# Kernel optimization log

Measured on AMD Instinct MI355X. Metric: run time of the kernel, lower is better.

Reference implementation:

```python
import jax, jax.numpy as jnp
import numpy as np

D_MODEL = 1024
N_HEAD = 8
STRIDE = 8
HEAD_DIM = D_MODEL // N_HEAD
NEG_INF = jnp.float32(-1e30)  # stand-in for -inf, safe under softmax


def setup_inputs() -> dict:
    key = jax.random.key(0)
    ks = jax.random.split(key, 8)
    B, TGT, SRC = 2, 1024, 8192
    scale = 1.0 / np.sqrt(D_MODEL)
    return {
        "q": jax.random.normal(ks[0], (B, TGT, D_MODEL), jnp.float32),
        "k": jax.random.normal(ks[1], (B, SRC, D_MODEL), jnp.float32),
        "v": jax.random.normal(ks[2], (B, SRC, D_MODEL), jnp.float32),
        "Wq": jax.random.normal(ks[3], (D_MODEL, D_MODEL), jnp.float32) * scale,
        "bq": jnp.zeros((D_MODEL,), jnp.float32),
        "Wk": jax.random.normal(ks[4], (D_MODEL, D_MODEL), jnp.float32) * scale,
        "bk": jnp.zeros((D_MODEL,), jnp.float32),
        "Wv": jax.random.normal(ks[5], (D_MODEL, D_MODEL), jnp.float32) * scale,
        "bv": jnp.zeros((D_MODEL,), jnp.float32),
        "Wo": jax.random.normal(ks[6], (D_MODEL, D_MODEL), jnp.float32) * scale,
        "bo": jnp.zeros((D_MODEL,), jnp.float32),
    }


def _hepos_head_mask(src_len):
    # mask_h[h, j] True where position j is DISALLOWED for head h:
    # (j - h) % stride != 0. If a head would mask everything, unmask j=0
    # (matches the torch fallback; cannot happen when n_head <= stride... it
    # can when h >= stride? here h < n_head <= stride handled generically).
    src_idx = jnp.arange(src_len)  # [src]
    h_idx = jnp.arange(N_HEAD)[:, None]  # [H,1]
    m = ((src_idx[None, :] - h_idx) % STRIDE) != 0  # [H, src]
    all_masked = jnp.all(m, axis=-1, keepdims=True)  # [H,1]
    m = m.at[:, 0].set(jnp.where(all_masked[:, 0], False, m[:, 0]))
    return m


def reference(q, k, v, Wq, bq, Wk, bk, Wv, bv, Wo, bo):
    B, tgt_len, _ = q.shape
    src_len = k.shape[1]
    # projections (torch Linear: x @ W^T + b; here W stored as [d_in, d_out])
    Q = (q @ Wq + bq).reshape(B, tgt_len, N_HEAD, HEAD_DIM)
    K = (k @ Wk + bk).reshape(B, src_len, N_HEAD, HEAD_DIM)
    V = (v @ Wv + bv).reshape(B, src_len, N_HEAD, HEAD_DIM)
    # dense scores [B, H, tgt, src]
    scores = jnp.einsum('bthd,bshd->bhts', Q, K) / np.sqrt(HEAD_DIM)
    head_mask = _hepos_head_mask(src_len)  # [H, src], True -> disallowed
    scores = jnp.where(head_mask[None, :, None, :], NEG_INF, scores)
    attn = jax.nn.softmax(scores, axis=-1)
    out = jnp.einsum('bhts,bshd->bthd', attn, V).reshape(B, tgt_len, D_MODEL)
    return out @ Wo + bo
```

## Files before the change

kernel.cpp:

```cpp
#include <hip/hip_runtime.h>
#include <hip/hip_bf16.h>
#include <stdint.h>

#define DM 1024
#define HD 128
#define NH 8
#define NB 2
#define TGT 1024
#define SRC 8192
#define JPH 1024
#define LOG2E 1.4426950408889634f

typedef __attribute__((ext_vector_type(8))) short bf16x8;
typedef __attribute__((ext_vector_type(4))) float f32x4;

__device__ __forceinline__ unsigned short f2bf(float f) {
  __hip_bfloat16 h = __float2bfloat16(f);
  return __builtin_bit_cast(unsigned short, h);
}

__device__ __forceinline__ void gload_lds16(const void* g, void* l) {
  __builtin_amdgcn_global_load_lds(
      (const __attribute__((address_space(1))) unsigned int*)g,
      (__attribute__((address_space(3))) unsigned int*)l, 16, 0, 0);
}

__global__ __launch_bounds__(256) void wconv_kernel(
    const float* __restrict__ Wq, const float* __restrict__ Wk,
    const float* __restrict__ Wv, const float* __restrict__ Wo,
    unsigned short* __restrict__ WTout) {
  __shared__ float tile[64][65];
  const float* W = (blockIdx.z == 0) ? Wq : (blockIdx.z == 1) ? Wk
                   : (blockIdx.z == 2) ? Wv : Wo;
  unsigned short* WT = WTout + (size_t)blockIdx.z * DM * DM;
  const int k0 = blockIdx.x * 64, n0 = blockIdx.y * 64;
  const int tid = threadIdx.x;
  const int tr = tid >> 4, tc = (tid & 15) * 4;
  for (int it = 0; it < 4; ++it) {
    int r = tr + it * 16;
    float4 vv = *(const float4*)(&W[(size_t)(k0 + r) * DM + n0 + tc]);
    tile[r][tc] = vv.x; tile[r][tc + 1] = vv.y;
    tile[r][tc + 2] = vv.z; tile[r][tc + 3] = vv.w;
  }
  __syncthreads();
  for (int it = 0; it < 4; ++it) {
    int n = tr + it * 16;
    ushort4 o;
    o.x = f2bf(tile[tc + 0][n]); o.y = f2bf(tile[tc + 1][n]);
    o.z = f2bf(tile[tc + 2][n]); o.w = f2bf(tile[tc + 3][n]);
    *(ushort4*)(&WT[(size_t)(n0 + n) * DM + k0 + tc]) = o;
  }
}

__global__ __launch_bounds__(256, 4) void proj_fused_kernel(
    const float* __restrict__ q, const float* __restrict__ k,
    const float* __restrict__ v, const unsigned short* __restrict__ WTall,
    const float* __restrict__ bq, const float* __restrict__ bk,
    const float* __restrict__ bv, unsigned short* __restrict__ Qp,
    unsigned short* __restrict__ Kp, unsigned short* __restrict__ VpT) {
  __shared__ unsigned short Ab[2][32 * 64];
  __shared__ unsigned short Bb[2][128 * 64];
  const int tid = threadIdx.x, lane = tid & 63, w = tid >> 6;
  const int wm = w >> 1, wn = w & 1;
  const int l15 = lane & 15, l4 = lane >> 4;

  const int bid = blockIdx.x;
  const int lbid = (bid & 7) * 192 + (bid >> 3);
  const int mode = lbid >> 9;
  const int sub = lbid & 511;
  const float* Asrc;
  const unsigned short* WT;
  const float* bias;
  int nbase, bh = 0, Mtile;
  if (mode == 0) {
    Asrc = q; WT = WTall; bias = bq;
    Mtile = sub >> 3; nbase = (sub & 7) * 128;
  } else {
    bh = sub >> 5; Mtile = sub & 31;
    nbase = (bh & 7) * 128;
    if (mode == 1) { Asrc = k; WT = WTall + (size_t)DM * DM; bias = bk; }
    else           { Asrc = v; WT = WTall + (size_t)2 * DM * DM; bias = bv; }
  }

  const int ar = tid >> 3;
  const int ac = (tid & 7) * 8;
  size_t growA;
  if (mode == 0) growA = (size_t)(Mtile * 32 + ar);
  else growA = (size_t)(bh >> 3) * SRC + (size_t)(bh & 7) +
               8u * (size_t)(Mtile * 32 + ar);
  const float* aptr = &Asrc[growA * DM + ac];

  auto issueA = [&](int t, float4 (&R)[2]) {
    const float* src = aptr + t * 64;
    R[0] = *(const float4*)(src);
    R[1] = *(const float4*)(src + 4);
  };
  auto commitA = [&](float4 (&R)[2], int buf) {
    bf16x8 pk;
    pk[0] = (short)f2bf(R[0].x); pk[1] = (short)f2bf(R[0].y);
    pk[2] = (short)f2bf(R[0].z); pk[3] = (short)f2bf(R[0].w);
    pk[4] = (short)f2bf(R[1].x); pk[5] = (short)f2bf(R[1].y);
    pk[6] = (short)f2bf(R[1].z); pk[7] = (short)f2bf(R[1].w);
    int b0 = ar * 128 + ((ac * 2) ^ ((ar & 7) << 4));
    *(bf16x8*)((unsigned char*)Ab[buf] + b0) = pk;
  };
  auto stageB = [&](int t, int buf) {
    const int kk0 = t * 64;
#pragma unroll
    for (int it = 0; it < 4; ++it) {
      int gi = w * 4 + it;
      int row = gi * 8 + (lane >> 3);
      const unsigned char* g =
          (const unsigned char*)&WT[(size_t)(nbase + row) * DM + kk0];
      g += ((lane & 7) * 16) ^ ((row & 7) << 4);
      gload_lds16(g, (unsigned char*)Bb[buf] + gi * 1024);
    }
  };

  f32x4 acc[4] = {};
  float4 aR0[2], aR1[2];

  stageB(0, 0);
  issueA(0, aR0);
  commitA(aR0, 0);
  issueA(1, aR1);
  asm volatile("s_waitcnt vmcnt(2) lgkmcnt(0)" ::: "memory");
  __builtin_amdgcn_s_barrier();
  __builtin_amdgcn_sched_barrier(0);

  auto body = [&](int T, int CUR, float4 (&RC)[2], float4 (&RN)[2]) {
    if (T + 1 < 16) stageB(T + 1, CUR ^ 1);
    if (T + 2 < 16) issueA(T + 2, RC);

    bf16x8 af[2], bfr[4][2];
#pragma unroll
    for (int kk = 0; kk < 2; ++kk) {
      int ra = wm * 16 + l15;
      int ka = (kk * 64 + l4 * 16) ^ ((ra & 7) << 4);
      af[kk] = *(const bf16x8*)((const unsigned char*)Ab[CUR] + ra * 128 + ka);
#pragma unroll
      for (int g = 0; g < 4; ++g) {
        int rb = wn * 64 + g * 16 + l15;
        int kb = (kk * 64 + l4 * 16) ^ ((rb & 7) << 4);
        bfr[g][kk] = *(const bf16x8*)((const unsigned char*)Bb[CUR] + rb * 128 + kb);
      }
    }
#pragma unroll
    for (int kk = 0; kk < 2; ++kk)
#pragma unroll
      for (int g = 0; g < 4; ++g)
        acc[g] = __builtin_amdgcn_mfma_f32_16x16x32_bf16(
            af[kk], bfr[g][kk], acc[g], 0, 0, 0);

    if (T + 1 < 16) commitA(RN, CUR ^ 1);

    if (T + 2 < 16)
      asm volatile("s_waitcnt vmcnt(2) lgkmcnt(0)" ::: "memory");
    else
      asm volatile("s_waitcnt vmcnt(0) lgkmcnt(0)" ::: "memory");
    __builtin_amdgcn_s_barrier();
    __builtin_amdgcn_sched_barrier(0);
  };

  for (int tt = 0; tt < 16; tt += 2) {
    body(tt, 0, aR0, aR1);
    body(tt + 1, 1, aR1, aR0);
  }

#pragma unroll
  for (int g = 0; g < 4; ++g) {
    const int mloc = wm * 16 + l4 * 4;
    const int nloc = wn * 64 + g * 16 + l15;
    const float bs = bias[nbase + nloc];
    if (mode == 2) {
      const int d = nloc;
      const int jp = Mtile * 32 + mloc;
      ushort4 o;
      o.x = f2bf(acc[g][0] + bs); o.y = f2bf(acc[g][1] + bs);
      o.z = f2bf(acc[g][2] + bs); o.w = f2bf(acc[g][3] + bs);
      *(ushort4*)(&VpT[((size_t)bh * HD + d) * JPH + jp]) = o;
    } else if (mode == 1) {
      for (int i = 0; i < 4; ++i) {
        int jp = Mtile * 32 + mloc + i;
        Kp[((size_t)bh * JPH + jp) * HD + nloc] = f2bf(acc[g][i] + bs);
      }
    } else {
      for (int i = 0; i < 4; ++i) {
        int mg = Mtile * 32 + mloc + i;
        int bb = mg >> 10, tt2 = mg & 1023;
        int ng = nbase + nloc;
        int h = ng >> 7, d = ng & 127;
        Qp[(((size_t)bb * NH + h) * TGT + tt2) * HD + d] =
            f2bf((acc[g][i] + bs) * 0.08838834764831845f);
      }
    }
  }
}

__global__ __launch_bounds__(256) void attn_kernel(
    const unsigned short* __restrict__ Qp, const unsigned short* __restrict__ Kp,
    const unsigned short* __restrict__ VpT, unsigned short* __restrict__ O) {
  __shared__ unsigned short Klds[2][64 * 128];
  __shared__ unsigned short Vlds[2][128 * 64];
  __shared__ unsigned short Plds[4 * 16 * 64];
  const int tid = threadIdx.x, lane = tid & 63, w = tid >> 6;
  const int bid = blockIdx.x;
  const int lbid = (bid & 7) * 32 + (bid >> 3);
  const int tq = lbid & 15, bh = lbid >> 4;
  const int T0 = tq * 64 + w * 16;
  const int l15 = lane & 15, l4 = lane >> 4;

  bf16x8 qf[4];
  {
    const unsigned short* qrow = &Qp[((size_t)bh * TGT + T0 + l15) * HD];
    for (int kf = 0; kf < 4; ++kf)
      qf[kf] = *(const bf16x8*)(&qrow[kf * 32 + l4 * 8]);
  }

  f32x4 acc_o[8] = {};
  float m_run = -INFINITY, l_run = 0.f;

  const unsigned short* kbh = Kp + (size_t)bh * JPH * HD;
  const unsigned short* vbh = VpT + (size_t)bh * HD * JPH;

  auto stage = [&](int jt, int buf) {
    const int j0 = jt * 64;
#pragma unroll
    for (int it = 0; it < 4; ++it) {
      int rb = w * 16 + it * 4;
      int row = rb + l4;
      const unsigned char* g =
          (const unsigned char*)(kbh + (size_t)(j0 + row) * HD);
      g += (l15 * 16) ^ ((row & 7) << 4);
      gload_lds16(g, &Klds[buf][rb * 128]);
    }
#pragma unroll
    for (int it = 0; it < 4; ++it) {
      int rb = w * 32 + it * 8;
      int d = rb + (lane >> 3);
      const unsigned char* g =
          (const unsigned char*)(vbh + (size_t)d * JPH + j0);
      g += ((lane & 7) * 16) ^ ((d & 7) << 4);
      gload_lds16(g, &Vlds[buf][rb * 64]);
    }
  };

  stage(0, 0);
  asm volatile("s_waitcnt vmcnt(0)" ::: "memory");
  __builtin_amdgcn_s_barrier();
  __builtin_amdgcn_sched_barrier(0);

  for (int jt = 0; jt < 16; ++jt) {
    const int cb = jt & 1;
    if (jt < 15) stage(jt + 1, cb ^ 1);

    f32x4 acc_s[4] = {};
    for (int jf = 0; jf < 4; ++jf) {
      const int j = jf * 16 + l15;
      for (int kf = 0; kf < 4; ++kf) {
        int byteoff = (j * 256 + (kf * 32 + l4 * 8) * 2) ^ ((j & 7) << 4);
        bf16x8 kfr = *(const bf16x8*)((const unsigned char*)Klds[cb] + byteoff);
        acc_s[jf] = __builtin_amdgcn_mfma_f32_16x16x32_bf16(
            kfr, qf[kf], acc_s[jf], 0, 0, 0);
      }
    }

    float pmax = -INFINITY;
    for (int jf = 0; jf < 4; ++jf)
      for (int i = 0; i < 4; ++i) pmax = fmaxf(pmax, acc_s[jf][i]);
    pmax = fmaxf(pmax, __shfl_xor(pmax, 16, 64));
    pmax = fmaxf(pmax, __shfl_xor(pmax, 32, 64));
    const float m_new = fmaxf(m_run, pmax);
    const float alpha = exp2f((m_run - m_new) * LOG2E);
    float psum = 0.f;
    for (int jf = 0; jf < 4; ++jf) {
      float p0 = exp2f((acc_s[jf][0] - m_new) * LOG2E);
      float p1 = exp2f((acc_s[jf][1] - m_new) * LOG2E);
      float p2 = exp2f((acc_s[jf][2] - m_new) * LOG2E);
      float p3 = exp2f((acc_s[jf][3] - m_new) * LOG2E);
      psum += (p0 + p1) + (p2 + p3);
      ushort4 pk;
      pk.x = f2bf(p0); pk.y = f2bf(p1); pk.z = f2bf(p2); pk.w = f2bf(p3);
      int byteoff = (w * 2048 + l15 * 128 + (jf * 16 + l4 * 4) * 2) ^ ((l15 & 7) << 4);
      *(ushort4*)((unsigned char*)Plds + byteoff) = pk;
    }
    psum += __shfl_xor(psum, 16, 64);
    psum += __shfl_xor(psum, 32, 64);
    l_run = l_run * alpha + psum;
    m_run = m_new;

    float alphar[4];
    for (int i = 0; i < 4; ++i)
      alphar[i] = __shfl(alpha, (lane & 48) | (l4 * 4 + i), 64);
    for (int df = 0; df < 8; ++df) {
      acc_o[df][0] *= alphar[0]; acc_o[df][1] *= alphar[1];
      acc_o[df][2] *= alphar[2]; acc_o[df][3] *= alphar[3];
    }

    for (int kf2 = 0; kf2 < 2; ++kf2) {
      int poff = (w * 2048 + l15 * 128 + (kf2 * 32 + l4 * 8) * 2) ^ ((l15 & 7) << 4);
      bf16x8 pf = *(const bf16x8*)((const unsigned char*)Plds + poff);
      for (int df = 0; df < 8; ++df) {
        int d = df * 16 + l15;
        int voff = (d * 128 + (kf2 * 32 + l4 * 8) * 2) ^ ((d & 7) << 4);
        bf16x8 vf = *(const bf16x8*)((const unsigned char*)Vlds[cb] + voff);
        acc_o[df] = __builtin_amdgcn_mfma_f32_16x16x32_bf16(
            pf, vf, acc_o[df], 0, 0, 0);
      }
    }

    asm volatile("s_waitcnt vmcnt(0)" ::: "memory");
    __builtin_amdgcn_s_barrier();
    __builtin_amdgcn_sched_barrier(0);
  }

  const float li = 1.0f / l_run;
  float linv[4];
  for (int i = 0; i < 4; ++i)
    linv[i] = __shfl(li, (lane & 48) | (l4 * 4 + i), 64);

  const int b = bh >> 3, h = bh & 7;
  for (int df = 0; df < 8; ++df)
    for (int i = 0; i < 4; ++i) {
      int t = T0 + l4 * 4 + i;
      int d = df * 16 + l15;
      O[((size_t)b * TGT + t) * DM + h * HD + d] = f2bf(acc_o[df][i] * linv[i]);
    }
}

__global__ __launch_bounds__(256) void oproj_kernel(
    const unsigned short* __restrict__ Oin, const unsigned short* __restrict__ WoT,
    const float* __restrict__ bo, float* __restrict__ out) {
  __shared__ unsigned short Ab[2][64 * 64];
  __shared__ unsigned short Bb[2][128 * 64];
  const int tid = threadIdx.x, lane = tid & 63, w = tid >> 6;
  const int wm = w >> 1, wn = w & 1;
  const int n0 = blockIdx.x * 128, m0 = blockIdx.y * 64;
  const int l15 = lane & 15, l4 = lane >> 4;

  auto stageA = [&](int t, int buf) {
    const int kk0 = t * 64;
#pragma unroll
    for (int it = 0; it < 2; ++it) {
      int gi = w * 2 + it;
      int row = gi * 8 + (lane >> 3);
      const unsigned char* g =
          (const unsigned char*)&Oin[(size_t)(m0 + row) * DM + kk0];
      g += ((lane & 7) * 16) ^ ((row & 7) << 4);
      gload_lds16(g, (unsigned char*)Ab[buf] + gi * 1024);
    }
  };
  auto stageB = [&](int t, int buf) {
    const int kk0 = t * 64;
#pragma unroll
    for (int it = 0; it < 4; ++it) {
      int gi = w * 4 + it;
      int row = gi * 8 + (lane >> 3);
      const unsigned char* g =
          (const unsigned char*)&WoT[(size_t)(n0 + row) * DM + kk0];
      g += ((lane & 7) * 16) ^ ((row & 7) << 4);
      gload_lds16(g, (unsigned char*)Bb[buf] + gi * 1024);
    }
  };

  f32x4 acc[2][4] = {};
  stageA(0, 0);
  stageB(0, 0);
  asm volatile("s_waitcnt vmcnt(0)" ::: "memory");
  __builtin_amdgcn_s_barrier();
  __builtin_amdgcn_sched_barrier(0);

  for (int t = 0; t < 16; ++t) {
    const int cur = t & 1;
    if (t < 15) { stageA(t + 1, cur ^ 1); stageB(t + 1, cur ^ 1); }

    bf16x8 af[2][2], bfr[4][2];
#pragma unroll
    for (int kk = 0; kk < 2; ++kk) {
#pragma unroll
      for (int f = 0; f < 2; ++f) {
        int ra = wm * 32 + f * 16 + l15;
        int ka = (kk * 64 + l4 * 16) ^ ((ra & 7) << 4);
        af[f][kk] = *(const bf16x8*)((const unsigned char*)Ab[cur] + ra * 128 + ka);
      }
#pragma unroll
      for (int g = 0; g < 4; ++g) {
        int rb = wn * 64 + g * 16 + l15;
        int kb = (kk * 64 + l4 * 16) ^ ((rb & 7) << 4);
        bfr[g][kk] = *(const bf16x8*)((const unsigned char*)Bb[cur] + rb * 128 + kb);
      }
    }
#pragma unroll
    for (int kk = 0; kk < 2; ++kk)
#pragma unroll
      for (int f = 0; f < 2; ++f)
#pragma unroll
        for (int g = 0; g < 4; ++g)
          acc[f][g] = __builtin_amdgcn_mfma_f32_16x16x32_bf16(
              af[f][kk], bfr[g][kk], acc[f][g], 0, 0, 0);

    asm volatile("s_waitcnt vmcnt(0) lgkmcnt(0)" ::: "memory");
    __builtin_amdgcn_s_barrier();
    __builtin_amdgcn_sched_barrier(0);
  }

#pragma unroll
  for (int f = 0; f < 2; ++f)
#pragma unroll
    for (int g = 0; g < 4; ++g) {
      int nn = n0 + wn * 64 + g * 16 + l15;
      float bs = bo[nn];
      for (int i = 0; i < 4; ++i) {
        int mm = m0 + wm * 32 + f * 16 + l4 * 4 + i;
        out[(size_t)mm * DM + nn] = acc[f][g][i] + bs;
      }
    }
}

extern "C" void kernel_launch(void* const* d_in, const int* in_sizes, int n_in,
                              void* d_out, int out_size, void* d_ws,
                              size_t ws_size, hipStream_t stream) {
  const float* q  = (const float*)d_in[0];
  const float* k  = (const float*)d_in[1];
  const float* v  = (const float*)d_in[2];
  const float* Wq = (const float*)d_in[3];
  const float* bq = (const float*)d_in[4];
  const float* Wk = (const float*)d_in[5];
  const float* bk = (const float*)d_in[6];
  const float* Wv = (const float*)d_in[7];
  const float* bv = (const float*)d_in[8];
  const float* Wo = (const float*)d_in[9];
  const float* bo = (const float*)d_in[10];
  float* out = (float*)d_out;

  unsigned short* WT  = (unsigned short*)d_ws;
  unsigned short* Qp  = WT + (size_t)4 * DM * DM;
  unsigned short* Kp  = Qp + (size_t)2 * DM * DM;
  unsigned short* VpT = Kp + (size_t)2 * DM * DM;
  unsigned short* Obf = VpT + (size_t)2 * DM * DM;

  hipLaunchKernelGGL(wconv_kernel, dim3(16, 16, 4), dim3(256), 0, stream,
                     Wq, Wk, Wv, Wo, WT);
  hipLaunchKernelGGL(proj_fused_kernel, dim3(1536), dim3(256), 0, stream,
                     q, k, v, WT, bq, bk, bv, Qp, Kp, VpT);
  hipLaunchKernelGGL(attn_kernel, dim3(256), dim3(256), 0, stream,
                     Qp, Kp, VpT, Obf);
  hipLaunchKernelGGL(oproj_kernel, dim3(8, 32), dim3(256), 0, stream,
                     Obf, WT + (size_t)3 * DM * DM, bo, out);
}
```

Before: 103.5 us.

## Double projection M-tile to 64 rows with triple-buffered B staging

The fused QKV projection kernel now computes 64x128 output tiles per block instead of 32x128, so each wave holds two MFMA row fragments and every staged weight tile is reused across twice as many rows. B staging moves from a double to a triple buffer with a two-tile prefetch distance, and the grid is halved to 768 blocks. Occupancy hints drop from 4 to 2 blocks per CU to allow the larger LDS and register footprint. The aim is to cut weight-tile traffic per output and hide more load latency, at the cost of fewer resident waves and fewer blocks to fill the GPU.

```diff
diff --git a/kernel.cpp b/kernel.cpp
--- a/kernel.cpp
+++ b/kernel.cpp
@@ -52,22 +52,22 @@
   }
 }
 
-__global__ __launch_bounds__(256, 4) void proj_fused_kernel(
+__global__ __launch_bounds__(256, 2) void proj_fused_kernel(
     const float* __restrict__ q, const float* __restrict__ k,
     const float* __restrict__ v, const unsigned short* __restrict__ WTall,
     const float* __restrict__ bq, const float* __restrict__ bk,
     const float* __restrict__ bv, unsigned short* __restrict__ Qp,
     unsigned short* __restrict__ Kp, unsigned short* __restrict__ VpT) {
-  __shared__ unsigned short Ab[2][32 * 64];
-  __shared__ unsigned short Bb[2][128 * 64];
+  __shared__ unsigned short Ab[2][64 * 64];
+  __shared__ unsigned short Bb[3][128 * 64];
   const int tid = threadIdx.x, lane = tid & 63, w = tid >> 6;
   const int wm = w >> 1, wn = w & 1;
   const int l15 = lane & 15, l4 = lane >> 4;
 
   const int bid = blockIdx.x;
-  const int lbid = (bid & 7) * 192 + (bid >> 3);
-  const int mode = lbid >> 9;
-  const int sub = lbid & 511;
+  const int lbid = (bid & 7) * 96 + (bid >> 3);
+  const int mode = lbid >> 8;
+  const int sub = lbid & 255;
   const float* Asrc;
   const unsigned short* WT;
   const float* bias;
@@ -76,36 +76,42 @@
     Asrc = q; WT = WTall; bias = bq;
     Mtile = sub >> 3; nbase = (sub & 7) * 128;
   } else {
-    bh = sub >> 5; Mtile = sub & 31;
+    bh = sub >> 4; Mtile = sub & 15;
     nbase = (bh & 7) * 128;
     if (mode == 1) { Asrc = k; WT = WTall + (size_t)DM * DM; bias = bk; }
     else           { Asrc = v; WT = WTall + (size_t)2 * DM * DM; bias = bv; }
   }
 
-  const int ar = tid >> 3;
-  const int ac = (tid & 7) * 8;
+  const int ar = tid >> 2;
+  const int ac = (tid & 3) * 16;
   size_t growA;
-  if (mode == 0) growA = (size_t)(Mtile * 32 + ar);
+  if (mode == 0) growA = (size_t)(Mtile * 64 + ar);
   else growA = (size_t)(bh >> 3) * SRC + (size_t)(bh & 7) +
-               8u * (size_t)(Mtile * 32 + ar);
+               8u * (size_t)(Mtile * 64 + ar);
   const float* aptr = &Asrc[growA * DM + ac];
 
-  auto issueA = [&](int t, float4 (&R)[2]) {
+  auto issueA = [&](int t, float4 (&R)[4]) {
     const float* src = aptr + t * 64;
-    R[0] = *(const float4*)(src);
-    R[1] = *(const float4*)(src + 4);
-  };
-  auto commitA = [&](float4 (&R)[2], int buf) {
-    bf16x8 pk;
-    pk[0] = (short)f2bf(R[0].x); pk[1] = (short)f2bf(R[0].y);
-    pk[2] = (short)f2bf(R[0].z); pk[3] = (short)f2bf(R[0].w);
-    pk[4] = (short)f2bf(R[1].x); pk[5] = (short)f2bf(R[1].y);
-    pk[6] = (short)f2bf(R[1].z); pk[7] = (short)f2bf(R[1].w);
-    int b0 = ar * 128 + ((ac * 2) ^ ((ar & 7) << 4));
-    *(bf16x8*)((unsigned char*)Ab[buf] + b0) = pk;
+#pragma unroll
+    for (int i = 0; i < 4; ++i) R[i] = *(const float4*)(src + i * 4);
+  };
+  auto commitA = [&](float4 (&R)[4], int buf) {
+    unsigned char* abase = (unsigned char*)Ab[buf] + ar * 128;
+#pragma unroll
+    for (int h = 0; h < 2; ++h) {
+      bf16x8 pk;
+      float4 x = R[h * 2], y = R[h * 2 + 1];
+      pk[0] = (short)f2bf(x.x); pk[1] = (short)f2bf(x.y);
+      pk[2] = (short)f2bf(x.z); pk[3] = (short)f2bf(x.w);
+      pk[4] = (short)f2bf(y.x); pk[5] = (short)f2bf(y.y);
+      pk[6] = (short)f2bf(y.z); pk[7] = (short)f2bf(y.w);
+      int b0 = (ac * 2 + h * 16) ^ ((ar & 7) << 4);
+      *(bf16x8*)(abase + b0) = pk;
+    }
   };
   auto stageB = [&](int t, int buf) {
     const int kk0 = t * 64;
+    unsigned char* dst = (unsigned char*)Bb[buf];
 #pragma unroll
     for (int it = 0; it < 4; ++it) {
       int gi = w * 4 + it;
@@ -113,85 +119,102 @@
       const unsigned char* g =
           (const unsigned char*)&WT[(size_t)(nbase + row) * DM + kk0];
       g += ((lane & 7) * 16) ^ ((row & 7) << 4);
-      gload_lds16(g, (unsigned char*)Bb[buf] + gi * 1024);
-    }
-  };
-
-  f32x4 acc[4] = {};
-  float4 aR0[2], aR1[2];
-
+      gload_lds16(g, dst + gi * 1024);
+    }
+  };
+
+  f32x4 acc[2][4] = {};
+  float4 aR0[4], aR1[4];
+
+  issueA(0, aR0);
   stageB(0, 0);
-  issueA(0, aR0);
+  issueA(1, aR1);
+  stageB(1, 1);
   commitA(aR0, 0);
-  issueA(1, aR1);
-  asm volatile("s_waitcnt vmcnt(2) lgkmcnt(0)" ::: "memory");
+  asm volatile("s_waitcnt vmcnt(8) lgkmcnt(0)" ::: "memory");
   __builtin_amdgcn_s_barrier();
   __builtin_amdgcn_sched_barrier(0);
 
-  auto body = [&](int T, int CUR, float4 (&RC)[2], float4 (&RN)[2]) {
-    if (T + 1 < 16) stageB(T + 1, CUR ^ 1);
-    if (T + 2 < 16) issueA(T + 2, RC);
-
-    bf16x8 af[2], bfr[4][2];
+  int bc = 0;
+
+  auto body = [&](int T, float4 (&RC)[4], float4 (&RN)[4]) {
+    int bp = bc + 2; if (bp >= 3) bp -= 3;
+    if (T + 2 < 16) {
+      issueA(T + 2, RC);
+      stageB(T + 2, bp);
+    }
+
+    const unsigned char* Bbase = (const unsigned char*)Bb[0] + bc * 16384;
+    const unsigned char* Abase = (const unsigned char*)Ab[T & 1];
+    bf16x8 af[2][2], bfr[4][2];
 #pragma unroll
     for (int kk = 0; kk < 2; ++kk) {
-      int ra = wm * 16 + l15;
-      int ka = (kk * 64 + l4 * 16) ^ ((ra & 7) << 4);
-      af[kk] = *(const bf16x8*)((const unsigned char*)Ab[CUR] + ra * 128 + ka);
+#pragma unroll
+      for (int f = 0; f < 2; ++f) {
+        int ra = wm * 32 + f * 16 + l15;
+        int ka = (kk * 64 + l4 * 16) ^ ((ra & 7) << 4);
+        af[f][kk] = *(const bf16x8*)(Abase + ra * 128 + ka);
+      }
 #pragma unroll
       for (int g = 0; g < 4; ++g) {
         int rb = wn * 64 + g * 16 + l15;
         int kb = (kk * 64 + l4 * 16) ^ ((rb & 7) << 4);
-        bfr[g][kk] = *(const bf16x8*)((const unsigned char*)Bb[CUR] + rb * 128 + kb);
+        bfr[g][kk] = *(const bf16x8*)(Bbase + rb * 128 + kb);
       }
     }
 #pragma unroll
     for (int kk = 0; kk < 2; ++kk)
 #pragma unroll
-      for (int g = 0; g < 4; ++g)
-        acc[g] = __builtin_amdgcn_mfma_f32_16x16x32_bf16(
-            af[kk], bfr[g][kk], acc[g], 0, 0, 0);
-
-    if (T + 1 < 16) commitA(RN, CUR ^ 1);
+      for (int f = 0; f < 2; ++f)
+#pragma unroll
+        for (int g = 0; g < 4; ++g)
+          acc[f][g] = __builtin_amdgcn_mfma_f32_16x16x32_bf16(
+              af[f][kk], bfr[g][kk], acc[f][g], 0, 0, 0);
+
+    if (T + 1 < 16) commitA(RN, (T + 1) & 1);
 
     if (T + 2 < 16)
-      asm volatile("s_waitcnt vmcnt(2) lgkmcnt(0)" ::: "memory");
+      asm volatile("s_waitcnt vmcnt(8) lgkmcnt(0)" ::: "memory");
     else
       asm volatile("s_waitcnt vmcnt(0) lgkmcnt(0)" ::: "memory");
     __builtin_amdgcn_s_barrier();
     __builtin_amdgcn_sched_barrier(0);
+    bc = bc + 1; if (bc >= 3) bc -= 3;
   };
 
   for (int tt = 0; tt < 16; tt += 2) {
-    body(tt, 0, aR0, aR1);
-    body(tt + 1, 1, aR1, aR0);
-  }
-
-#pragma unroll
-  for (int g = 0; g < 4; ++g) {
-    const int mloc = wm * 16 + l4 * 4;
-    const int nloc = wn * 64 + g * 16 + l15;
-    const float bs = bias[nbase + nloc];
-    if (mode == 2) {
-      const int d = nloc;
-      const int jp = Mtile * 32 + mloc;
-      ushort4 o;
-      o.x = f2bf(acc[g][0] + bs); o.y = f2bf(acc[g][1] + bs);
-      o.z = f2bf(acc[g][2] + bs); o.w = f2bf(acc[g][3] + bs);
-      *(ushort4*)(&VpT[((size_t)bh * HD + d) * JPH + jp]) = o;
-    } else if (mode == 1) {
-      for (int i = 0; i < 4; ++i) {
-        int jp = Mtile * 32 + mloc + i;
-        Kp[((size_t)bh * JPH + jp) * HD + nloc] = f2bf(acc[g][i] + bs);
-      }
-    } else {
-      for (int i = 0; i < 4; ++i) {
-        int mg = Mtile * 32 + mloc + i;
-        int bb = mg >> 10, tt2 = mg & 1023;
-        int ng = nbase + nloc;
-        int h = ng >> 7, d = ng & 127;
-        Qp[(((size_t)bb * NH + h) * TGT + tt2) * HD + d] =
-            f2bf((acc[g][i] + bs) * 0.08838834764831845f);
+    body(tt, aR0, aR1);
+    body(tt + 1, aR1, aR0);
+  }
+
+#pragma unroll
+  for (int f = 0; f < 2; ++f) {
+#pragma unroll
+    for (int g = 0; g < 4; ++g) {
+      const int mloc = wm * 32 + f * 16 + l4 * 4;
+      const int nloc = wn * 64 + g * 16 + l15;
+      const float bs = bias[nbase + nloc];
+      if (mode == 2) {
+        const int d = nloc;
+        const int jp = Mtile * 64 + mloc;
+        ushort4 o;
+        o.x = f2bf(acc[f][g][0] + bs); o.y = f2bf(acc[f][g][1] + bs);
+        o.z = f2bf(acc[f][g][2] + bs); o.w = f2bf(acc[f][g][3] + bs);
+        *(ushort4*)(&VpT[((size_t)bh * HD + d) * JPH + jp]) = o;
+      } else if (mode == 1) {
+        for (int i = 0; i < 4; ++i) {
+          int jp = Mtile * 64 + mloc + i;
+          Kp[((size_t)bh * JPH + jp) * HD + nloc] = f2bf(acc[f][g][i] + bs);
+        }
+      } else {
+        for (int i = 0; i < 4; ++i) {
+          int mg = Mtile * 64 + mloc + i;
+          int bb = mg >> 10, tt2 = mg & 1023;
+          int ng = nbase + nloc;
+          int h = ng >> 7, d = ng & 127;
+          Qp[(((size_t)bb * NH + h) * TGT + tt2) * HD + d] =
+              f2bf((acc[f][g][i] + bs) * 0.08838834764831845f);
+        }
       }
     }
   }
@@ -441,7 +464,7 @@
 
   hipLaunchKernelGGL(wconv_kernel, dim3(16, 16, 4), dim3(256), 0, stream,
                      Wq, Wk, Wv, Wo, WT);
-  hipLaunchKernelGGL(proj_fused_kernel, dim3(1536), dim3(256), 0, stream,
+  hipLaunchKernelGGL(proj_fused_kernel, dim3(768), dim3(256), 0, stream,
                      q, k, v, WT, bq, bk, bv, Qp, Kp, VpT);
   hipLaunchKernelGGL(attn_kernel, dim3(256), dim3(256), 0, stream,
                      Qp, Kp, VpT, Obf);
```

Measured after the change: 106.2 us. 1.03x slower.
